# Kernel tuning notes

Hardware: AMD Instinct MI355X
Metric: run time of the kernel (lower is better)

## Reference

```python
import jax, jax.numpy as jnp
import numpy as np

B, LQ, LK = 2, 2048, 77
DIM, XDIM = 320, 768
H, HD = 8, 40  # heads, head_dim; DIM == H*HD
FF = 4 * DIM  # GEGLU inner dim


def _ln(x, g, b, eps=1e-5):
    m = x.mean(-1, keepdims=True)
    v = ((x - m) ** 2).mean(-1, keepdims=True)
    return (x - m) * jax.lax.rsqrt(v + eps) * g + b


def _split_heads(x):  # [B,L,DIM] -> [B,H,L,HD]
    return x.reshape(x.shape[0], x.shape[1], H, HD).transpose(0, 2, 1, 3)


def _merge_heads(x):  # [B,H,L,HD] -> [B,L,DIM]
    return x.transpose(0, 2, 1, 3).reshape(x.shape[0], x.shape[2], H * HD)


def setup_inputs() -> dict:
    key = jax.random.key(0)
    ks = jax.random.split(key, 24)
    s = 0.02
    r = lambda i, shp: s * jax.random.normal(ks[i], shp, jnp.float32)
    return {
        "hidden_states": jax.random.normal(ks[0], (B, LQ, DIM), jnp.float32),
        "encoder_hidden_states": jax.random.normal(ks[1], (B, LK, XDIM), jnp.float32),
        # norm1 + self-attn (attn1)
        "ln1_g": jnp.ones((DIM,), jnp.float32), "ln1_b": jnp.zeros((DIM,), jnp.float32),
        "wq1": r(2, (DIM, DIM)), "wk1": r(3, (DIM, DIM)), "wv1": r(4, (DIM, DIM)),
        "wo1": r(5, (DIM, DIM)), "bo1": jnp.zeros((DIM,), jnp.float32),
        # norm2 + Hadamard cross-attn (attn2)
        "ln2_g": jnp.ones((DIM,), jnp.float32), "ln2_b": jnp.zeros((DIM,), jnp.float32),
        "wq2": r(6, (DIM, DIM)), "wk2": r(7, (XDIM, DIM)), "wvh": r(8, (DIM, DIM)),
        "wo2": r(9, (DIM, DIM)), "bo2": jnp.zeros((DIM,), jnp.float32),
        # norm3 + GEGLU feed-forward
        "ln3_g": jnp.ones((DIM,), jnp.float32), "ln3_b": jnp.zeros((DIM,), jnp.float32),
        "wff1": r(10, (DIM, 2 * FF)), "bff1": jnp.zeros((2 * FF,), jnp.float32),
        "wff2": r(11, (FF, DIM)), "bff2": jnp.zeros((DIM,), jnp.float32),
    }


def reference(hidden_states, encoder_hidden_states, ln1_g, ln1_b, wq1, wk1, wv1,
              wo1, bo1, ln2_g, ln2_b, wq2, wk2, wvh, wo2, bo2, ln3_g, ln3_b,
              wff1, bff1, wff2, bff2):
    scale = 1.0 / jnp.sqrt(jnp.asarray(HD, hidden_states.dtype))

    # ---- self-attention (SDPA semantics) ----
    h = _ln(hidden_states, ln1_g, ln1_b)
    q = _split_heads(h @ wq1)
    k = _split_heads(h @ wk1)
    v = _split_heads(h @ wv1)
    scores = jnp.einsum('bhqd,bhkd->bhqk', q, k) * scale
    w = jax.nn.softmax(scores, axis=-1)
    attn = jnp.einsum('bhqk,bhkd->bhqd', w, v)
    attn = _merge_heads(attn) @ wo1 + bo1
    hidden_states = hidden_states + attn

    # ---- Hadamard cross-attention: value comes from hidden_states (len Lq) ----
    h = _ln(hidden_states, ln2_g, ln2_b)
    q = _split_heads(h @ wq2)                     # [B,H,Lq,HD]
    k = _split_heads(encoder_hidden_states @ wk2) # [B,H,Lk,HD]
    vH = _split_heads(h @ wvh)                    # [B,H,Lq,HD]
    scores = jnp.einsum('bhqd,bhkd->bhqk', q, k) * scale
    w = jax.nn.softmax(scores, axis=-1)           # [B,H,Lq,Lk]
    # (w[...,None] * vH[...,None,:]).sum(-2) == vH * w.sum(-1, keepdims) (v indep of k)
    cross = vH * jnp.sum(w, axis=-1, keepdims=True)
    cross = _merge_heads(cross) @ wo2 + bo2
    hidden_states = hidden_states + cross

    # ---- GEGLU feed-forward ----
    h = _ln(hidden_states, ln3_g, ln3_b)
    proj = h @ wff1 + bff1
    x, gate = jnp.split(proj, 2, axis=-1)
    ff = (x * jax.nn.gelu(gate, approximate=False)) @ wff2 + bff2
    return hidden_states + ff
```

## Files before the change

kernel.cpp:

```cpp
#include <hip/hip_runtime.h>
#include <math.h>

#define DIM   320
#define HD    40
#define NH    8
#define LQ    2048
#define BATCH 2
#define MROWS 4096
#define FFD   1280
#define FF2   2560

#define KSPLIT 4
#define KCHUNK (LQ/KSPLIT)
#define KT     32
#define NT     (KCHUNK/KT)
#define NQROWS (BATCH*NH*LQ)

#define LSCALE (0.15811388300841897f * 1.4426950408889634f)

typedef unsigned short ushort_t;
typedef unsigned int u32;
using bf16x8 = __attribute__((ext_vector_type(8))) short;
using f32x4  = __attribute__((ext_vector_type(4))) float;

#define AS1 __attribute__((address_space(1)))
#define AS3 __attribute__((address_space(3)))

static __device__ inline ushort_t f2bf(float f) {
  union { float f; unsigned u; } x{f};
  unsigned r = x.u + 0x7FFFu + ((x.u >> 16) & 1u);
  return (ushort_t)(r >> 16);
}
static __device__ inline float bf2f(ushort_t h) {
  union { unsigned u; float f; } x; x.u = ((unsigned)h) << 16; return x.f;
}

__global__ __launch_bounds__(256) void ln_kernel(
    const float* __restrict__ X, const float* __restrict__ g,
    const float* __restrict__ bta, ushort_t* __restrict__ Y)
{
  int row  = blockIdx.x * 4 + (threadIdx.x >> 6);
  int lane = threadIdx.x & 63;
  const float* x = X + (size_t)row * DIM;
  float v[5];
  float s = 0.f;
#pragma unroll
  for (int i = 0; i < 5; ++i) { v[i] = x[lane + 64*i]; s += v[i]; }
#pragma unroll
  for (int off = 32; off >= 1; off >>= 1) s += __shfl_xor(s, off, 64);
  float mean = s * (1.0f/DIM);
  float sq = 0.f;
#pragma unroll
  for (int i = 0; i < 5; ++i) { float d = v[i] - mean; sq += d*d; }
#pragma unroll
  for (int off = 32; off >= 1; off >>= 1) sq += __shfl_xor(sq, off, 64);
  float rstd = rsqrtf(sq*(1.0f/DIM) + 1e-5f);
  ushort_t* y = Y + (size_t)row * DIM;
#pragma unroll
  for (int i = 0; i < 5; ++i) {
    int c = lane + 64*i;
    y[c] = f2bf((v[i]-mean)*rstd*g[c] + bta[c]);
  }
}

#define OFF_WQKVT 0
#define OFF_WO1T  (960*320)
#define OFF_WO2T  (OFF_WO1T + 320*320)
#define OFF_WFF1T (OFF_WO2T + 320*320)
#define OFF_WFF2T (OFF_WFF1T + 320*2560)
#define OFF_WVHB  (OFF_WFF2T + 1280*320)
#define WBF_TOTAL (OFF_WVHB + 320*320)

__global__ __launch_bounds__(256) void convw_kernel(
    const float* __restrict__ wq1, const float* __restrict__ wk1,
    const float* __restrict__ wv1, const float* __restrict__ wo1,
    const float* __restrict__ wo2, const float* __restrict__ wff1,
    const float* __restrict__ wff2, const float* __restrict__ wvh,
    ushort_t* __restrict__ dst, ushort_t* __restrict__ Kimg)
{
  int e = blockIdx.y;
  if (e == 8) {
    int f = blockIdx.x*256 + threadIdx.x;
    if (f < 98304) {
      int g3 = f/3, cidx = f - 3*g3;
      int rr = g3 & 31, tile = (g3 >> 5) & 63, bh = g3 >> 11;
      uint4 z = {0,0,0,0};
      *(uint4*)(Kimg + ((size_t)(bh*64 + tile))*2048 + rr*64
                + (((5+cidx) ^ (rr&7)) << 3)) = z;
    }
    return;
  }
  const float* src; int K, N; size_t doff; int tr = 1; float scale = 1.f;
  switch (e) {
    case 0: src=wq1;  K=320;  N=320;  doff=OFF_WQKVT; scale=LSCALE; break;
    case 1: src=wk1;  K=320;  N=320;  doff=OFF_WQKVT + 320*320;  break;
    case 2: src=wv1;  K=320;  N=320;  doff=OFF_WQKVT + 2*320*320;break;
    case 3: src=wo1;  K=320;  N=320;  doff=OFF_WO1T;             break;
    case 4: src=wo2;  K=320;  N=320;  doff=OFF_WO2T;             break;
    case 5: src=wff1; K=320;  N=2560; doff=OFF_WFF1T;            break;
    case 6: src=wff2; K=1280; N=320;  doff=OFF_WFF2T;            break;
    default: src=wvh; K=320;  N=320;  doff=OFF_WVHB; tr=0;       break;
  }
  int ntN = N/32;
  int nt_total = (K/32)*ntN;
  int t = blockIdx.x;
  if (t >= nt_total) return;
  int kt = t / ntN, nt = t - kt*ntN;
  __shared__ float tile[32][33];
  int tx = threadIdx.x & 31, ty = threadIdx.x >> 5;
  ushort_t* d = dst + doff;
#pragma unroll
  for (int i = 0; i < 4; ++i) {
    int r = ty + 8*i;
    tile[r][tx] = src[(size_t)(kt*32+r)*N + nt*32+tx] * scale;
  }
  __syncthreads();
  if (tr) {
#pragma unroll
    for (int i = 0; i < 4; ++i) {
      int r = ty + 8*i;
      d[(size_t)(nt*32+r)*K + kt*32+tx] = f2bf(tile[tx][r]);
    }
  } else {
#pragma unroll
    for (int i = 0; i < 4; ++i) {
      int r = ty + 8*i;
      d[(size_t)(kt*32+r)*N + nt*32+tx] = f2bf(tile[r][tx]);
    }
  }
}

#define AST 72
__global__ __launch_bounds__(256) void mgemm(
    const ushort_t* __restrict__ A, int lda,
    const ushort_t* __restrict__ Bt, int ldb,
    const float* __restrict__ bias,
    const float* __restrict__ R,
    float* __restrict__ Cf, ushort_t* __restrict__ Cb, int ldc,
    int K)
{
  __shared__ ushort_t As[64*AST];
  __shared__ ushort_t Bs[64*AST];
  int tid = threadIdx.x;
  int w = tid >> 6, lane = tid & 63, quad = lane >> 4, n16 = lane & 15;
  int wm = w >> 1, wn = w & 1;
  int bm = blockIdx.y * 64, bn = blockIdx.x * 64;
  int sr = tid >> 2, sc = (tid & 3) << 4;
  const ushort_t* Ag = A  + (size_t)(bm + sr)*lda + sc;
  const ushort_t* Bg = Bt + (size_t)(bn + sr)*ldb + sc;

  f32x4 acc00 = {0.f,0.f,0.f,0.f}, acc01 = acc00, acc10 = acc00, acc11 = acc00;

  float4 av0 = *(const float4*)(Ag);
  float4 av1 = *(const float4*)(Ag + 8);
  float4 bv0 = *(const float4*)(Bg);
  float4 bv1 = *(const float4*)(Bg + 8);
  for (int k0 = 0; k0 < K; k0 += 64) {
    __syncthreads();
    *(float4*)(As + sr*AST + sc)     = av0;
    *(float4*)(As + sr*AST + sc + 8) = av1;
    *(float4*)(Bs + sr*AST + sc)     = bv0;
    *(float4*)(Bs + sr*AST + sc + 8) = bv1;
    __syncthreads();
    if (k0 + 64 < K) {
      av0 = *(const float4*)(Ag + k0 + 64);
      av1 = *(const float4*)(Ag + k0 + 72);
      bv0 = *(const float4*)(Bg + k0 + 64);
      bv1 = *(const float4*)(Bg + k0 + 72);
    }
#pragma unroll
    for (int kk = 0; kk < 64; kk += 32) {
      bf16x8 fa0 = *(const bf16x8*)(As + (wm*32 +      n16)*AST + kk + quad*8);
      bf16x8 fa1 = *(const bf16x8*)(As + (wm*32 + 16 + n16)*AST + kk + quad*8);
      bf16x8 fb0 = *(const bf16x8*)(Bs + (wn*32 +      n16)*AST + kk + quad*8);
      bf16x8 fb1 = *(const bf16x8*)(Bs + (wn*32 + 16 + n16)*AST + kk + quad*8);
      acc00 = __builtin_amdgcn_mfma_f32_16x16x32_bf16(fa0, fb0, acc00, 0,0,0);
      acc01 = __builtin_amdgcn_mfma_f32_16x16x32_bf16(fa0, fb1, acc01, 0,0,0);
      acc10 = __builtin_amdgcn_mfma_f32_16x16x32_bf16(fa1, fb0, acc10, 0,0,0);
      acc11 = __builtin_amdgcn_mfma_f32_16x16x32_bf16(fa1, fb1, acc11, 0,0,0);
    }
  }

  f32x4 accs[2][2] = {{acc00, acc01},{acc10, acc11}};
#pragma unroll
  for (int s = 0; s < 2; ++s)
#pragma unroll
    for (int t = 0; t < 2; ++t) {
      int c = bn + wn*32 + t*16 + n16;
      float bb = bias ? bias[c] : 0.f;
#pragma unroll
      for (int i = 0; i < 4; ++i) {
        int r = bm + wm*32 + s*16 + quad*4 + i;
        float v = accs[s][t][i] + bb;
        if (R)  v += R[(size_t)r*ldc + c];
        if (Cf) Cf[(size_t)r*ldc + c] = v;
        if (Cb) Cb[(size_t)r*ldc + c] = f2bf(v);
      }
    }
}

__global__ __launch_bounds__(256) void mgemm128_qkv(
    const ushort_t* __restrict__ A, const ushort_t* __restrict__ Bt,
    ushort_t* __restrict__ Qb, ushort_t* __restrict__ Kimg,
    ushort_t* __restrict__ Vimg)
{
  __shared__ ushort_t As[128*AST];
  __shared__ ushort_t Bs[64*AST];
  int tid = threadIdx.x;
  int w = tid >> 6, lane = tid & 63, quad = lane >> 4, n16 = lane & 15;
  int wm = w >> 1, wn = w & 1;
  int bm = blockIdx.y * 128, bn = blockIdx.x * 64;
  int ar = tid >> 2, ac = (tid & 3) << 4;
  const ushort_t* Ag0 = A  + (size_t)(bm + ar)*DIM + ac;
  const ushort_t* Ag1 = A  + (size_t)(bm + 64 + ar)*DIM + ac;
  const ushort_t* Bg  = Bt + (size_t)(bn + ar)*DIM + ac;

  f32x4 acc[4][2];
#pragma unroll
  for (int s = 0; s < 4; ++s)
#pragma unroll
    for (int t = 0; t < 2; ++t) acc[s][t] = f32x4{0.f,0.f,0.f,0.f};

  float4 a00 = *(const float4*)(Ag0);
  float4 a01 = *(const float4*)(Ag0 + 8);
  float4 a10 = *(const float4*)(Ag1);
  float4 a11 = *(const float4*)(Ag1 + 8);
  float4 b0  = *(const float4*)(Bg);
  float4 b1  = *(const float4*)(Bg + 8);
  for (int k0 = 0; k0 < DIM; k0 += 64) {
    __syncthreads();
    *(float4*)(As + ar*AST + ac)          = a00;
    *(float4*)(As + ar*AST + ac + 8)      = a01;
    *(float4*)(As + (64+ar)*AST + ac)     = a10;
    *(float4*)(As + (64+ar)*AST + ac + 8) = a11;
    *(float4*)(Bs + ar*AST + ac)          = b0;
    *(float4*)(Bs + ar*AST + ac + 8)      = b1;
    __syncthreads();
    if (k0 + 64 < DIM) {
      a00 = *(const float4*)(Ag0 + k0 + 64);
      a01 = *(const float4*)(Ag0 + k0 + 72);
      a10 = *(const float4*)(Ag1 + k0 + 64);
      a11 = *(const float4*)(Ag1 + k0 + 72);
      b0  = *(const float4*)(Bg  + k0 + 64);
      b1  = *(const float4*)(Bg  + k0 + 72);
    }
#pragma unroll
    for (int kk = 0; kk < 64; kk += 32) {
      bf16x8 fa[4], fb[2];
#pragma unroll
      for (int s = 0; s < 4; ++s)
        fa[s] = *(const bf16x8*)(As + (wm*64 + s*16 + n16)*AST + kk + quad*8);
#pragma unroll
      for (int t = 0; t < 2; ++t)
        fb[t] = *(const bf16x8*)(Bs + (wn*32 + t*16 + n16)*AST + kk + quad*8);
#pragma unroll
      for (int s = 0; s < 4; ++s)
#pragma unroll
        for (int t = 0; t < 2; ++t)
          acc[s][t] = __builtin_amdgcn_mfma_f32_16x16x32_bf16(fa[s], fb[t], acc[s][t], 0,0,0);
    }
  }

  int b8 = (bm >> 11) << 3;
  if (bn < 320) {
#pragma unroll
    for (int s = 0; s < 4; ++s)
#pragma unroll
      for (int t = 0; t < 2; ++t) {
        int c = bn + wn*32 + t*16 + n16;
#pragma unroll
        for (int i = 0; i < 4; ++i) {
          int r = bm + wm*64 + s*16 + quad*4 + i;
          Qb[(size_t)r*320 + c] = f2bf(acc[s][t][i]);
        }
      }
  } else if (bn < 640) {
#pragma unroll
    for (int t = 0; t < 2; ++t) {
      int c = bn + wn*32 + t*16 + n16 - 320;
      int hK = c / 40, d = c - hK*40;
#pragma unroll
      for (int s = 0; s < 4; ++s)
#pragma unroll
        for (int i = 0; i < 4; ++i) {
          int r = bm + wm*64 + s*16 + quad*4 + i;
          int l = r & 2047, tl = l >> 5, rr = l & 31;
          Kimg[((size_t)((b8 + hK)*64 + tl))*2048 + rr*64
               + (((d >> 3) ^ (rr & 7)) << 3) + (d & 7)] = f2bf(acc[s][t][i]);
        }
    }
  } else {
#pragma unroll
    for (int t = 0; t < 2; ++t) {
      int c = bn + wn*32 + t*16 + n16 - 640;
      int hV = c / 40, d = c - hV*40;
#pragma unroll
      for (int s = 0; s < 4; ++s) {
        int l0 = (bm + wm*64 + s*16 + quad*4) & 2047;
        int tl = l0 >> 5, p0 = (l0 & 31) >> 1;
        ushort_t* vb = Vimg + ((size_t)((b8 + hV)*64 + tl))*1536 + d*32;
#pragma unroll
        for (int j = 0; j < 2; ++j) {
          int p = p0 + j;
          unsigned val = (unsigned)f2bf(acc[s][t][2*j])
                       | ((unsigned)f2bf(acc[s][t][2*j+1]) << 16);
          *(unsigned*)(vb + (((p >> 2) ^ (d & 3)) << 3) + ((p & 3) << 1)) = val;
        }
      }
    }
  }
}

__global__ __launch_bounds__(256) void ff1_geglu(
    const ushort_t* __restrict__ A, const ushort_t* __restrict__ Bt,
    const float* __restrict__ bias, ushort_t* __restrict__ Og)
{
  __shared__ ushort_t As[128*AST];
  __shared__ ushort_t Bxs[64*AST];
  __shared__ ushort_t Bgs[64*AST];
  int tid = threadIdx.x;
  int w = tid >> 6, lane = tid & 63, quad = lane >> 4, n16 = lane & 15;
  int wm = w >> 1, wn = w & 1;
  int bm = blockIdx.y * 128, bn = blockIdx.x * 64;
  int ar = tid >> 2, ac = (tid & 3) << 4;
  const ushort_t* Ag0 = A  + (size_t)(bm + ar)*DIM + ac;
  const ushort_t* Ag1 = A  + (size_t)(bm + 64 + ar)*DIM + ac;
  const ushort_t* Bxg = Bt + (size_t)(bn + ar)*DIM + ac;
  const ushort_t* Bgg = Bt + (size_t)(bn + FFD + ar)*DIM + ac;

  f32x4 ax[4][2], ag[4][2];
#pragma unroll
  for (int s = 0; s < 4; ++s)
#pragma unroll
    for (int t = 0; t < 2; ++t) { ax[s][t] = f32x4{0.f,0.f,0.f,0.f}; ag[s][t] = ax[s][t]; }

  float4 a00 = *(const float4*)(Ag0);
  float4 a01 = *(const float4*)(Ag0 + 8);
  float4 a10 = *(const float4*)(Ag1);
  float4 a11 = *(const float4*)(Ag1 + 8);
  float4 bx0 = *(const float4*)(Bxg);
  float4 bx1 = *(const float4*)(Bxg + 8);
  float4 bg0 = *(const float4*)(Bgg);
  float4 bg1 = *(const float4*)(Bgg + 8);
  for (int k0 = 0; k0 < DIM; k0 += 64) {
    __syncthreads();
    *(float4*)(As  + ar*AST + ac)          = a00;
    *(float4*)(As  + ar*AST + ac + 8)      = a01;
    *(float4*)(As  + (64+ar)*AST + ac)     = a10;
    *(float4*)(As  + (64+ar)*AST + ac + 8) = a11;
    *(float4*)(Bxs + ar*AST + ac)          = bx0;
    *(float4*)(Bxs + ar*AST + ac + 8)      = bx1;
    *(float4*)(Bgs + ar*AST + ac)          = bg0;
    *(float4*)(Bgs + ar*AST + ac + 8)      = bg1;
    __syncthreads();
    if (k0 + 64 < DIM) {
      a00 = *(const float4*)(Ag0 + k0 + 64);
      a01 = *(const float4*)(Ag0 + k0 + 72);
      a10 = *(const float4*)(Ag1 + k0 + 64);
      a11 = *(const float4*)(Ag1 + k0 + 72);
      bx0 = *(const float4*)(Bxg + k0 + 64);
      bx1 = *(const float4*)(Bxg + k0 + 72);
      bg0 = *(const float4*)(Bgg + k0 + 64);
      bg1 = *(const float4*)(Bgg + k0 + 72);
    }
#pragma unroll
    for (int kk = 0; kk < 64; kk += 32) {
      bf16x8 fa[4], fx[2], fg[2];
#pragma unroll
      for (int s = 0; s < 4; ++s)
        fa[s] = *(const bf16x8*)(As + (wm*64 + s*16 + n16)*AST + kk + quad*8);
#pragma unroll
      for (int t = 0; t < 2; ++t) {
        fx[t] = *(const bf16x8*)(Bxs + (wn*32 + t*16 + n16)*AST + kk + quad*8);
        fg[t] = *(const bf16x8*)(Bgs + (wn*32 + t*16 + n16)*AST + kk + quad*8);
      }
#pragma unroll
      for (int s = 0; s < 4; ++s)
#pragma unroll
        for (int t = 0; t < 2; ++t) {
          ax[s][t] = __builtin_amdgcn_mfma_f32_16x16x32_bf16(fa[s], fx[t], ax[s][t], 0,0,0);
          ag[s][t] = __builtin_amdgcn_mfma_f32_16x16x32_bf16(fa[s], fg[t], ag[s][t], 0,0,0);
        }
    }
  }

  const float kk2 = 0.7071067811865476f;
#pragma unroll
  for (int s = 0; s < 4; ++s)
#pragma unroll
    for (int t = 0; t < 2; ++t) {
      int c = bn + wn*32 + t*16 + n16;
      float bx = bias[c], bg = bias[c + FFD];
#pragma unroll
      for (int i = 0; i < 4; ++i) {
        int r = bm + wm*64 + s*16 + quad*4 + i;
        float xx = ax[s][t][i] + bx;
        float gg = ag[s][t][i] + bg;
        Og[(size_t)r*FFD + c] = f2bf(xx * 0.5f * gg * (1.f + erff(gg * kk2)));
      }
    }
}

#define TILE_K_SH 2048
#define TILE_V_SH 1536
#define TILE_SH   (TILE_K_SH + TILE_V_SH)

__global__ __launch_bounds__(256, 2) void attn_mfma(
    const ushort_t* __restrict__ Qb, const ushort_t* __restrict__ Kimg,
    const ushort_t* __restrict__ Vimg,
    float* __restrict__ Pl, ushort_t* __restrict__ Pacc)
{
  __shared__ ushort_t lds[4*TILE_SH];
  int tid  = threadIdx.x;
  int w    = tid >> 6;
  int lane = tid & 63;
  int quad = lane >> 4;
  int n16  = lane & 15;

  int blk  = blockIdx.x;
  int bh   = (blk & 7) | (((blk >> 3) & 1) << 3);
  int rest = blk >> 4;
  int qt   = rest & 15;
  int ks   = rest >> 4;
  int b = bh >> 3, h = bh & 7;

  const ushort_t* qrowa = Qb + (size_t)(b*LQ + qt*128 + w*32 + n16)*320 + h*HD;
  const ushort_t* qrowb = qrowa + 16*320;
  bf16x8 qf0a = *(const bf16x8*)(qrowa + quad*8);
  bf16x8 qf1a = *(const bf16x8*)(qrowa + 32);
  bf16x8 qf0b = *(const bf16x8*)(qrowb + quad*8);
  bf16x8 qf1b = *(const bf16x8*)(qrowb + 32);

  const ushort_t* Ktb = Kimg + ((size_t)bh*64 + ks*NT)*TILE_K_SH;
  const ushort_t* Vtb = Vimg + ((size_t)bh*64 + ks*NT)*TILE_V_SH;

  int swk0 = (quad ^ (n16 & 7)) << 3;
  int swk1 = ((quad + 4) ^ (n16 & 7)) << 3;
  int kof0 = n16*64 + swk0;
  int kof1 = n16*64 + swk1;
  int kof2 = (16+n16)*64 + swk0;
  int kof3 = (16+n16)*64 + swk1;
  int swv  = (quad ^ (n16 & 3)) << 3;
  int vof0 = n16*32 + swv;
  int vof1 = (16+n16)*32 + swv;
  int vof2 = (32+n16)*32 + swv;

  f32x4 o0a = {0.f,0.f,0.f,0.f}, o1a = o0a, o2a = o0a;
  f32x4 o0b = o0a, o1b = o0a, o2b = o0a;
  f32x4 la0a = o0a, la1a = o0a, la0b = o0a, la1b = o0a;

#define CVTPK(D, LO, HI) \
  asm("v_cvt_pk_bf16_f32 %0, %1, %2" : "=v"(D) : "v"(LO), "v"(HI))
#define PSWAP32(X, Y) \
  asm("v_permlane32_swap_b32 %0, %1" : "+v"(X), "+v"(Y))
#define PSWAP16(X, Y) \
  asm("v_permlane16_swap_b32 %0, %1" : "+v"(X), "+v"(Y))

#define STAGE(SLOT, T) { \
  const ushort_t* ks_ = Ktb + (size_t)(T)*TILE_K_SH + w*512 + lane*8; \
  ushort_t* kd_ = lds + (SLOT)*TILE_SH + w*512; \
  __builtin_amdgcn_global_load_lds( \
      (const AS1 u32*)ks_, (AS3 u32*)kd_, 16, 0, 0); \
  if (w < 3) { \
    const ushort_t* vs_ = Vtb + (size_t)(T)*TILE_V_SH + w*512 + lane*8; \
    ushort_t* vd_ = lds + (SLOT)*TILE_SH + TILE_K_SH + w*512; \
    __builtin_amdgcn_global_load_lds( \
        (const AS1 u32*)vs_, (AS3 u32*)vd_, 16, 0, 0); \
  } }

#define HALF(Q0F, Q1F, LA0, LA1, FRAG) \
  bf16x8 FRAG; { \
  f32x4 st0 = {-8.f,-8.f,-8.f,-8.f}; f32x4 st1 = st0; \
  st0 = __builtin_amdgcn_mfma_f32_16x16x32_bf16(K00, Q0F, st0, 0,0,0); \
  st1 = __builtin_amdgcn_mfma_f32_16x16x32_bf16(K10, Q0F, st1, 0,0,0); \
  st0 = __builtin_amdgcn_mfma_f32_16x16x32_bf16(K01, Q1F, st0, 0,0,0); \
  st1 = __builtin_amdgcn_mfma_f32_16x16x32_bf16(K11, Q1F, st1, 0,0,0); \
  f32x4 p0, p1; \
  _Pragma("unroll") \
  for (int r = 0; r < 4; ++r) { p0[r] = exp2f(st0[r]); p1[r] = exp2f(st1[r]); } \
  LA0 += p0; LA1 += p1; \
  unsigned d0, d1, d2, d3; \
  CVTPK(d0, p0[0], p0[1]); CVTPK(d1, p0[2], p0[3]); \
  CVTPK(d2, p1[0], p1[1]); CVTPK(d3, p1[2], p1[3]); \
  PSWAP32(d0, d2); PSWAP16(d0, d2); \
  PSWAP32(d1, d3); PSWAP16(d1, d3); \
  union { unsigned u[4]; bf16x8 v; } fr_; \
  fr_.u[0] = d0; fr_.u[1] = d1; fr_.u[2] = d2; fr_.u[3] = d3; \
  FRAG = fr_.v; }

#define CTILE(SLOT) { \
  const ushort_t* Kb_ = lds + (SLOT)*TILE_SH; \
  const ushort_t* Vb_ = Kb_ + TILE_K_SH; \
  bf16x8 K00 = *(const bf16x8*)(Kb_ + kof0); \
  bf16x8 K01 = *(const bf16x8*)(Kb_ + kof1); \
  bf16x8 K10 = *(const bf16x8*)(Kb_ + kof2); \
  bf16x8 K11 = *(const bf16x8*)(Kb_ + kof3); \
  bf16x8 V0  = *(const bf16x8*)(Vb_ + vof0); \
  bf16x8 V1  = *(const bf16x8*)(Vb_ + vof1); \
  bf16x8 V2  = *(const bf16x8*)(Vb_ + vof2); \
  HALF(qf0a, qf1a, la0a, la1a, fragA) \
  HALF(qf0b, qf1b, la0b, la1b, fragB) \
  o0a = __builtin_amdgcn_mfma_f32_16x16x32_bf16(fragA, V0, o0a, 0,0,0); \
  o0b = __builtin_amdgcn_mfma_f32_16x16x32_bf16(fragB, V0, o0b, 0,0,0); \
  o1a = __builtin_amdgcn_mfma_f32_16x16x32_bf16(fragA, V1, o1a, 0,0,0); \
  o1b = __builtin_amdgcn_mfma_f32_16x16x32_bf16(fragB, V1, o1b, 0,0,0); \
  o2a = __builtin_amdgcn_mfma_f32_16x16x32_bf16(fragA, V2, o2a, 0,0,0); \
  o2b = __builtin_amdgcn_mfma_f32_16x16x32_bf16(fragB, V2, o2b, 0,0,0); }

  STAGE(0, 0); STAGE(1, 1);
  __syncthreads();
  for (int s = 0; s < NT/2; ++s) {
    int sb = s & 1;
    if (s + 1 < NT/2) {
      STAGE((sb^1)*2,     2*s + 2);
      STAGE((sb^1)*2 + 1, 2*s + 3);
    }
    CTILE(sb*2);
    CTILE(sb*2 + 1);
    __syncthreads();
  }
#undef STAGE
#undef CTILE
#undef HALF
#undef CVTPK
#undef PSWAP32
#undef PSWAP16

  float sA = la0a[0]+la0a[1]+la0a[2]+la0a[3] + la1a[0]+la1a[1]+la1a[2]+la1a[3];
  float sB = la0b[0]+la0b[1]+la0b[2]+la0b[3] + la1b[0]+la1b[1]+la1b[2]+la1b[3];
  sA += __shfl_xor(sA, 16, 64); sA += __shfl_xor(sA, 32, 64);
  sB += __shfl_xor(sB, 16, 64); sB += __shfl_xor(sB, 32, 64);

  int grow = bh*LQ + qt*128 + w*32;
  size_t base = (size_t)ks*NQROWS;
  if (lane < 16) {
    Pl[base + grow + n16]      = sA;
    Pl[base + grow + 16 + n16] = sB;
  }

  int gqa = grow + quad*4;
#pragma unroll
  for (int r = 0; r < 4; ++r) {
    size_t gq = base + gqa + r;
    ushort_t* pw = Pacc + gq*40;
    pw[n16]      = f2bf(o0a[r]);
    pw[16 + n16] = f2bf(o1a[r]);
    if (n16 < 8) pw[32 + n16] = f2bf(o2a[r]);
    size_t gq2 = gq + 16;
    ushort_t* pw2 = Pacc + gq2*40;
    pw2[n16]      = f2bf(o0b[r]);
    pw2[16 + n16] = f2bf(o1b[r]);
    if (n16 < 8) pw2[32 + n16] = f2bf(o2b[r]);
  }
}

__global__ __launch_bounds__(256) void attn_merge(
    const float* __restrict__ Pl, const ushort_t* __restrict__ Pacc,
    ushort_t* __restrict__ O)
{
  int t = blockIdx.x*256 + threadIdx.x;
  int idx = t / 5;
  int u   = t - idx*5;
  int bh = idx >> 11, qi = idx & (LQ-1);
  int b = bh >> 3, h = bh & 7;
  float L = 0.f;
#pragma unroll
  for (int k = 0; k < KSPLIT; ++k) L += Pl[(size_t)k*NQROWS + idx];
  float inv = 1.0f / L;
  float acc[8] = {0,0,0,0,0,0,0,0};
#pragma unroll
  for (int k = 0; k < KSPLIT; ++k) {
    const ushort_t* pr = Pacc + ((size_t)k*NQROWS + idx)*40 + u*8;
    ushort_t vbuf[8];
    *(uint4*)vbuf = *(const uint4*)pr;
#pragma unroll
    for (int j = 0; j < 8; ++j) acc[j] += bf2f(vbuf[j]);
  }
  ushort_t ob[8];
#pragma unroll
  for (int j = 0; j < 8; ++j) ob[j] = f2bf(acc[j]*inv);
  ushort_t* orow = O + (size_t)(b*LQ + qi)*DIM + h*HD;
  *(uint4*)(orow + u*8) = *(uint4*)ob;
}

extern "C" void kernel_launch(void* const* d_in, const int* in_sizes, int n_in,
                              void* d_out, int out_size, void* d_ws, size_t ws_size,
                              hipStream_t stream) {
  const float* hidden = (const float*)d_in[0];
  const float* ln1_g = (const float*)d_in[2];
  const float* ln1_b = (const float*)d_in[3];
  const float* wq1   = (const float*)d_in[4];
  const float* wk1   = (const float*)d_in[5];
  const float* wv1   = (const float*)d_in[6];
  const float* wo1   = (const float*)d_in[7];
  const float* bo1   = (const float*)d_in[8];
  const float* ln2_g = (const float*)d_in[9];
  const float* ln2_b = (const float*)d_in[10];
  const float* wvh   = (const float*)d_in[13];
  const float* wo2   = (const float*)d_in[14];
  const float* bo2   = (const float*)d_in[15];
  const float* ln3_g = (const float*)d_in[16];
  const float* ln3_b = (const float*)d_in[17];
  const float* wff1  = (const float*)d_in[18];
  const float* bff1  = (const float*)d_in[19];
  const float* wff2  = (const float*)d_in[20];
  const float* bff2  = (const float*)d_in[21];
  float* out = (float*)d_out;

  ushort_t* wsu = (ushort_t*)d_ws;
  ushort_t* wbf   = wsu;
  ushort_t* lnb   = wbf + WBF_TOTAL;
  ushort_t* Qb    = lnb + (size_t)MROWS*DIM;
  ushort_t* attnb = Qb + (size_t)MROWS*DIM;
  ushort_t* gegb  = attnb + (size_t)MROWS*DIM;
  ushort_t* wct   = gegb + (size_t)MROWS*FFD;
  ushort_t* vtb   = wct + 320*320;
  ushort_t* kpb   = vtb + (size_t)16*64*1536;
  ushort_t* Pacc  = kpb + (size_t)16*64*2048;
  float* fws = (float*)((((uintptr_t)(Pacc + (size_t)KSPLIT*NQROWS*40)) + 255) & ~(uintptr_t)255);
  float* h1   = fws;
  float* h2   = h1 + (size_t)MROWS*DIM;
  float* Pl   = h2 + (size_t)MROWS*DIM;

  dim3 t256(256);
  dim3 gconv(1024, 9);
  dim3 gqkv(15, 32);
  dim3 g320(5, 64);
  dim3 gwc(5, 5);
  dim3 gffg(20, 32);
  dim3 gattn(16*16*KSPLIT);

  convw_kernel<<<gconv, t256, 0, stream>>>(wq1, wk1, wv1, wo1, wo2, wff1, wff2,
                                           wvh, wbf, kpb);
  mgemm<<<gwc, t256, 0, stream>>>(wbf + OFF_WO2T, DIM, wbf + OFF_WVHB, DIM,
                                  nullptr, nullptr, nullptr, wct, DIM, DIM);

  ln_kernel<<<MROWS/4, t256, 0, stream>>>(hidden, ln1_g, ln1_b, lnb);
  mgemm128_qkv<<<gqkv, t256, 0, stream>>>(lnb, wbf + OFF_WQKVT, Qb, kpb, vtb);
  attn_mfma<<<gattn, t256, 0, stream>>>(Qb, kpb, vtb, Pl, Pacc);
  attn_merge<<<NQROWS*5/256, t256, 0, stream>>>(Pl, Pacc, attnb);
  mgemm<<<g320, t256, 0, stream>>>(attnb, DIM, wbf + OFF_WO1T, DIM, bo1, hidden,
                                   h1, nullptr, DIM, DIM);

  ln_kernel<<<MROWS/4, t256, 0, stream>>>(h1, ln2_g, ln2_b, lnb);
  mgemm<<<g320, t256, 0, stream>>>(lnb, DIM, wct, DIM, bo2, h1,
                                   h2, nullptr, DIM, DIM);

  ln_kernel<<<MROWS/4, t256, 0, stream>>>(h2, ln3_g, ln3_b, lnb);
  ff1_geglu<<<gffg, t256, 0, stream>>>(lnb, wbf + OFF_WFF1T, bff1, gegb);
  mgemm<<<g320, t256, 0, stream>>>(gegb, FFD, wbf + OFF_WFF2T, FFD, bff2, h2,
                                   out, nullptr, DIM, FFD);
}
```

Before: 209.9 us.

## Fuse LN2, cross projection GEMM and LN3 into one kernel; fold LN1 into convw

Merges the ln1 launch into the weight-conversion kernel as an extra grid slice. It also replaces the LN2 → Wc GEMM → LN3 sequence with one row-block kernel that normalizes h1 into LDS and streams a pre-swizzled Wc via global_load_lds. The epilogue then adds bias and residual, writes h2, and computes LN3 in-block. A dedicated wc_gemm writes the combined weight in the swizzled layout. This removes three launches and the round trips of the intermediate LN outputs. The trade-offs are a one-pass variance formula and a grid of only 16-row blocks, each re-streaming all of Wc.

Measured after the change: 202.4 us. -3.6%, faster.

```diff
diff --git a/kernel.cpp b/kernel.cpp
--- a/kernel.cpp
+++ b/kernel.cpp
@@ -35,34 +35,6 @@
   union { unsigned u; float f; } x; x.u = ((unsigned)h) << 16; return x.f;
 }
 
-__global__ __launch_bounds__(256) void ln_kernel(
-    const float* __restrict__ X, const float* __restrict__ g,
-    const float* __restrict__ bta, ushort_t* __restrict__ Y)
-{
-  int row  = blockIdx.x * 4 + (threadIdx.x >> 6);
-  int lane = threadIdx.x & 63;
-  const float* x = X + (size_t)row * DIM;
-  float v[5];
-  float s = 0.f;
-#pragma unroll
-  for (int i = 0; i < 5; ++i) { v[i] = x[lane + 64*i]; s += v[i]; }
-#pragma unroll
-  for (int off = 32; off >= 1; off >>= 1) s += __shfl_xor(s, off, 64);
-  float mean = s * (1.0f/DIM);
-  float sq = 0.f;
-#pragma unroll
-  for (int i = 0; i < 5; ++i) { float d = v[i] - mean; sq += d*d; }
-#pragma unroll
-  for (int off = 32; off >= 1; off >>= 1) sq += __shfl_xor(sq, off, 64);
-  float rstd = rsqrtf(sq*(1.0f/DIM) + 1e-5f);
-  ushort_t* y = Y + (size_t)row * DIM;
-#pragma unroll
-  for (int i = 0; i < 5; ++i) {
-    int c = lane + 64*i;
-    y[c] = f2bf((v[i]-mean)*rstd*g[c] + bta[c]);
-  }
-}
-
 #define OFF_WQKVT 0
 #define OFF_WO1T  (960*320)
 #define OFF_WO2T  (OFF_WO1T + 320*320)
@@ -76,7 +48,9 @@
     const float* __restrict__ wv1, const float* __restrict__ wo1,
     const float* __restrict__ wo2, const float* __restrict__ wff1,
     const float* __restrict__ wff2, const float* __restrict__ wvh,
-    ushort_t* __restrict__ dst, ushort_t* __restrict__ Kimg)
+    ushort_t* __restrict__ dst, ushort_t* __restrict__ Kimg,
+    const float* __restrict__ hidden, const float* __restrict__ ln1_g,
+    const float* __restrict__ ln1_b, ushort_t* __restrict__ lnb)
 {
   int e = blockIdx.y;
   if (e == 8) {
@@ -87,6 +61,31 @@
       uint4 z = {0,0,0,0};
       *(uint4*)(Kimg + ((size_t)(bh*64 + tile))*2048 + rr*64
                 + (((5+cidx) ^ (rr&7)) << 3)) = z;
+    }
+    return;
+  }
+  if (e == 9) {
+    int row  = blockIdx.x * 4 + (threadIdx.x >> 6);
+    int lane = threadIdx.x & 63;
+    const float* x = hidden + (size_t)row * DIM;
+    float v[5];
+    float s = 0.f;
+#pragma unroll
+    for (int i = 0; i < 5; ++i) { v[i] = x[lane + 64*i]; s += v[i]; }
+#pragma unroll
+    for (int off = 32; off >= 1; off >>= 1) s += __shfl_xor(s, off, 64);
+    float mean = s * (1.0f/DIM);
+    float sq = 0.f;
+#pragma unroll
+    for (int i = 0; i < 5; ++i) { float d = v[i] - mean; sq += d*d; }
+#pragma unroll
+    for (int off = 32; off >= 1; off >>= 1) sq += __shfl_xor(sq, off, 64);
+    float rstd = rsqrtf(sq*(1.0f/DIM) + 1e-5f);
+    ushort_t* y = lnb + (size_t)row * DIM;
+#pragma unroll
+    for (int i = 0; i < 5; ++i) {
+      int c = lane + 64*i;
+      y[c] = f2bf((v[i]-mean)*rstd*ln1_g[c] + ln1_b[c]);
     }
     return;
   }
@@ -197,6 +196,199 @@
         if (Cb) Cb[(size_t)r*ldc + c] = f2bf(v);
       }
     }
+}
+
+__global__ __launch_bounds__(256) void wc_gemm(
+    const ushort_t* __restrict__ A, const ushort_t* __restrict__ Bt,
+    ushort_t* __restrict__ Wctb)
+{
+  __shared__ ushort_t As[64*AST];
+  __shared__ ushort_t Bs[64*AST];
+  int tid = threadIdx.x;
+  int w = tid >> 6, lane = tid & 63, quad = lane >> 4, n16 = lane & 15;
+  int wm = w >> 1, wn = w & 1;
+  int bm = blockIdx.y * 64, bn = blockIdx.x * 64;
+  int sr = tid >> 2, sc = (tid & 3) << 4;
+  const ushort_t* Ag = A  + (size_t)(bm + sr)*DIM + sc;
+  const ushort_t* Bg = Bt + (size_t)(bn + sr)*DIM + sc;
+
+  f32x4 acc00 = {0.f,0.f,0.f,0.f}, acc01 = acc00, acc10 = acc00, acc11 = acc00;
+
+  float4 av0 = *(const float4*)(Ag);
+  float4 av1 = *(const float4*)(Ag + 8);
+  float4 bv0 = *(const float4*)(Bg);
+  float4 bv1 = *(const float4*)(Bg + 8);
+  for (int k0 = 0; k0 < DIM; k0 += 64) {
+    __syncthreads();
+    *(float4*)(As + sr*AST + sc)     = av0;
+    *(float4*)(As + sr*AST + sc + 8) = av1;
+    *(float4*)(Bs + sr*AST + sc)     = bv0;
+    *(float4*)(Bs + sr*AST + sc + 8) = bv1;
+    __syncthreads();
+    if (k0 + 64 < DIM) {
+      av0 = *(const float4*)(Ag + k0 + 64);
+      av1 = *(const float4*)(Ag + k0 + 72);
+      bv0 = *(const float4*)(Bg + k0 + 64);
+      bv1 = *(const float4*)(Bg + k0 + 72);
+    }
+#pragma unroll
+    for (int kk = 0; kk < 64; kk += 32) {
+      bf16x8 fa0 = *(const bf16x8*)(As + (wm*32 +      n16)*AST + kk + quad*8);
+      bf16x8 fa1 = *(const bf16x8*)(As + (wm*32 + 16 + n16)*AST + kk + quad*8);
+      bf16x8 fb0 = *(const bf16x8*)(Bs + (wn*32 +      n16)*AST + kk + quad*8);
+      bf16x8 fb1 = *(const bf16x8*)(Bs + (wn*32 + 16 + n16)*AST + kk + quad*8);
+      acc00 = __builtin_amdgcn_mfma_f32_16x16x32_bf16(fa0, fb0, acc00, 0,0,0);
+      acc01 = __builtin_amdgcn_mfma_f32_16x16x32_bf16(fa0, fb1, acc01, 0,0,0);
+      acc10 = __builtin_amdgcn_mfma_f32_16x16x32_bf16(fa1, fb0, acc10, 0,0,0);
+      acc11 = __builtin_amdgcn_mfma_f32_16x16x32_bf16(fa1, fb1, acc11, 0,0,0);
+    }
+  }
+
+  f32x4 accs[2][2] = {{acc00, acc01},{acc10, acc11}};
+#pragma unroll
+  for (int s = 0; s < 2; ++s)
+#pragma unroll
+    for (int t = 0; t < 2; ++t) {
+      int c = bn + wn*32 + t*16 + n16;
+#pragma unroll
+      for (int i = 0; i < 4; ++i) {
+        int r = bm + wm*32 + s*16 + quad*4 + i;
+        Wctb[((size_t)(c >> 5)*320 + r)*32
+             + ((((c >> 3) & 3) ^ (r & 3)) << 3) + (c & 7)] = f2bf(accs[s][t][i]);
+      }
+    }
+}
+
+__global__ __launch_bounds__(256) void cross_ln(
+    const float* __restrict__ h1,
+    const float* __restrict__ g2, const float* __restrict__ b2,
+    const ushort_t* __restrict__ Wctb,
+    const float* __restrict__ bo2,
+    const float* __restrict__ g3, const float* __restrict__ b3,
+    float* __restrict__ h2, ushort_t* __restrict__ lnb)
+{
+  __shared__ ushort_t Asm[16*328];
+  __shared__ ushort_t Bsm[2*10240];
+  __shared__ float    sred[4][16][2];
+  __shared__ float    fstat[16][2];
+  int tid = threadIdx.x;
+  int w = tid >> 6, lane = tid & 63, quad = lane >> 4, n16 = lane & 15;
+  int r0 = blockIdx.x * 16;
+
+  int ar = tid >> 4;
+  int aj = tid & 15;
+  {
+    const float* hrow = h1 + (size_t)(r0 + ar)*DIM + aj*20;
+    float xv[20];
+    float s = 0.f, q = 0.f;
+#pragma unroll
+    for (int i = 0; i < 5; ++i) {
+      float4 v = *(const float4*)(hrow + 4*i);
+      xv[4*i]=v.x; xv[4*i+1]=v.y; xv[4*i+2]=v.z; xv[4*i+3]=v.w;
+      s += v.x+v.y+v.z+v.w;
+      q += v.x*v.x+v.y*v.y+v.z*v.z+v.w*v.w;
+    }
+#pragma unroll
+    for (int off = 1; off < 16; off <<= 1) {
+      s += __shfl_xor(s, off, 64);
+      q += __shfl_xor(q, off, 64);
+    }
+    float m_  = s*(1.f/DIM);
+    float rs_ = rsqrtf(fmaxf(q*(1.f/DIM) - m_*m_, 0.f) + 1e-5f);
+    float gg[20], bb[20];
+#pragma unroll
+    for (int i = 0; i < 5; ++i) {
+      *(float4*)(gg+4*i) = *(const float4*)(g2 + aj*20 + 4*i);
+      *(float4*)(bb+4*i) = *(const float4*)(b2 + aj*20 + 4*i);
+    }
+    ushort_t tb[20];
+#pragma unroll
+    for (int j = 0; j < 20; ++j)
+      tb[j] = f2bf((xv[j]-m_)*rs_*gg[j] + bb[j]);
+#pragma unroll
+    for (int i = 0; i < 5; ++i)
+      *(uint2*)(Asm + ar*328 + aj*20 + 4*i) = *(uint2*)(tb + 4*i);
+  }
+
+#define STAGEB(BUF, KB) { \
+  const ushort_t* src_ = Wctb + (size_t)(KB)*10240; \
+  _Pragma("unroll") \
+  for (int i = 0; i < 5; ++i) { \
+    __builtin_amdgcn_global_load_lds( \
+        (const AS1 u32*)(src_ + i*2048 + w*512 + lane*8), \
+        (AS3 u32*)(Bsm + (BUF)*10240 + i*2048 + w*512), 16, 0, 0); \
+  } }
+
+  f32x4 acc[5];
+#pragma unroll
+  for (int t = 0; t < 5; ++t) acc[t] = f32x4{0.f,0.f,0.f,0.f};
+
+  STAGEB(0, 0);
+  __syncthreads();
+  int bbuf = 0;
+  for (int kb = 0; kb < 10; ++kb) {
+    if (kb + 1 < 10) STAGEB(bbuf^1, kb + 1);
+    const ushort_t* Bb = Bsm + bbuf*10240;
+    bf16x8 fa = *(const bf16x8*)(Asm + n16*328 + kb*32 + quad*8);
+#pragma unroll
+    for (int t = 0; t < 5; ++t) {
+      int c = w*80 + t*16 + n16;
+      bf16x8 fb = *(const bf16x8*)(Bb + c*32 + ((quad ^ (c & 3)) << 3));
+      acc[t] = __builtin_amdgcn_mfma_f32_16x16x32_bf16(fa, fb, acc[t], 0,0,0);
+    }
+    __syncthreads();
+    bbuf ^= 1;
+  }
+#undef STAGEB
+
+  float hv[5][4];
+  float ss[4] = {0,0,0,0}, qq[4] = {0,0,0,0};
+#pragma unroll
+  for (int t = 0; t < 5; ++t) {
+    int c = w*80 + t*16 + n16;
+    float bb = bo2[c];
+#pragma unroll
+    for (int i = 0; i < 4; ++i) {
+      int r = r0 + quad*4 + i;
+      float v = acc[t][i] + bb + h1[(size_t)r*DIM + c];
+      hv[t][i] = v;
+      h2[(size_t)r*DIM + c] = v;
+      ss[i] += v; qq[i] += v*v;
+    }
+  }
+#pragma unroll
+  for (int off = 1; off < 16; off <<= 1)
+#pragma unroll
+    for (int i = 0; i < 4; ++i) {
+      ss[i] += __shfl_xor(ss[i], off, 64);
+      qq[i] += __shfl_xor(qq[i], off, 64);
+    }
+  if (n16 == 0)
+#pragma unroll
+    for (int i = 0; i < 4; ++i) {
+      sred[w][quad*4 + i][0] = ss[i];
+      sred[w][quad*4 + i][1] = qq[i];
+    }
+  __syncthreads();
+  if (tid < 16) {
+    float S = sred[0][tid][0]+sred[1][tid][0]+sred[2][tid][0]+sred[3][tid][0];
+    float Q = sred[0][tid][1]+sred[1][tid][1]+sred[2][tid][1]+sred[3][tid][1];
+    float mm = S*(1.f/DIM);
+    fstat[tid][0] = mm;
+    fstat[tid][1] = rsqrtf(fmaxf(Q*(1.f/DIM) - mm*mm, 0.f) + 1e-5f);
+  }
+  __syncthreads();
+#pragma unroll
+  for (int t = 0; t < 5; ++t) {
+    int c = w*80 + t*16 + n16;
+    float gg = g3[c], bb = b3[c];
+#pragma unroll
+    for (int i = 0; i < 4; ++i) {
+      int rr = quad*4 + i;
+      lnb[(size_t)(r0 + rr)*DIM + c] =
+          f2bf((hv[t][i] - fstat[rr][0])*fstat[rr][1]*gg + bb);
+    }
+  }
 }
 
 __global__ __launch_bounds__(256) void mgemm128_qkv(
@@ -623,7 +815,7 @@
   float* Pl   = h2 + (size_t)MROWS*DIM;
 
   dim3 t256(256);
-  dim3 gconv(1024, 9);
+  dim3 gconv(1024, 10);
   dim3 gqkv(15, 32);
   dim3 g320(5, 64);
   dim3 gwc(5, 5);
@@ -631,22 +823,18 @@
   dim3 gattn(16*16*KSPLIT);
 
   convw_kernel<<<gconv, t256, 0, stream>>>(wq1, wk1, wv1, wo1, wo2, wff1, wff2,
-                                           wvh, wbf, kpb);
-  mgemm<<<gwc, t256, 0, stream>>>(wbf + OFF_WO2T, DIM, wbf + OFF_WVHB, DIM,
-                                  nullptr, nullptr, nullptr, wct, DIM, DIM);
-
-  ln_kernel<<<MROWS/4, t256, 0, stream>>>(hidden, ln1_g, ln1_b, lnb);
+                                           wvh, wbf, kpb, hidden, ln1_g, ln1_b, lnb);
+  wc_gemm<<<gwc, t256, 0, stream>>>(wbf + OFF_WO2T, wbf + OFF_WVHB, wct);
+
   mgemm128_qkv<<<gqkv, t256, 0, stream>>>(lnb, wbf + OFF_WQKVT, Qb, kpb, vtb);
   attn_mfma<<<gattn, t256, 0, stream>>>(Qb, kpb, vtb, Pl, Pacc);
   attn_merge<<<NQROWS*5/256, t256, 0, stream>>>(Pl, Pacc, attnb);
   mgemm<<<g320, t256, 0, stream>>>(attnb, DIM, wbf + OFF_WO1T, DIM, bo1, hidden,
                                    h1, nullptr, DIM, DIM);
 
-  ln_kernel<<<MROWS/4, t256, 0, stream>>>(h1, ln2_g, ln2_b, lnb);
-  mgemm<<<g320, t256, 0, stream>>>(lnb, DIM, wct, DIM, bo2, h1,
-                                   h2, nullptr, DIM, DIM);
-
-  ln_kernel<<<MROWS/4, t256, 0, stream>>>(h2, ln3_g, ln3_b, lnb);
+  cross_ln<<<MROWS/16, t256, 0, stream>>>(h1, ln2_g, ln2_b, wct, bo2,
+                                          ln3_g, ln3_b, h2, lnb);
+
   ff1_geglu<<<gffg, t256, 0, stream>>>(lnb, wbf + OFF_WFF1T, bff1, gegb);
   mgemm<<<g320, t256, 0, stream>>>(gegb, FFD, wbf + OFF_WFF2T, FFD, bff2, h2,
                                    out, nullptr, DIM, FFD);
```
